# Kernel optimization log

Hardware: AMD Instinct MI355X
Metric: run time of the kernel (lower is better)

Reference implementation:

```python
import jax, jax.numpy as jnp
import numpy as np

B, T, C = 4, 2048, 1024
H = 16
HD = C // H

def setup_inputs() -> dict:
    key = jax.random.key(0)
    k1, k2, k3 = jax.random.split(key, 3)
    x = jax.random.normal(k1, (B, T, C), dtype=jnp.float32)
    w_attn = jax.random.normal(k2, (C, 3 * C), dtype=jnp.float32) * 0.02
    b_attn = jnp.zeros((3 * C,), dtype=jnp.float32)
    w_proj = jax.random.normal(k3, (C, C), dtype=jnp.float32) * 0.02
    b_proj = jnp.zeros((C,), dtype=jnp.float32)
    return {"x": x, "w_attn": w_attn, "b_attn": b_attn, "w_proj": w_proj, "b_proj": b_proj}

def reference(x, w_attn, b_attn, w_proj, b_proj):
    Bx, Tx, Cx = x.shape
    qkv = x @ w_attn + b_attn                      # [B,T,3C]
    q, k, v = jnp.split(qkv, 3, axis=-1)
    # [B,T,C] -> [B,H,T,HD]
    q = q.reshape(Bx, Tx, H, HD).transpose(0, 2, 1, 3)
    k = k.reshape(Bx, Tx, H, HD).transpose(0, 2, 1, 3)
    v = v.reshape(Bx, Tx, H, HD).transpose(0, 2, 1, 3)
    scale = 1.0 / jnp.sqrt(jnp.asarray(HD, dtype=x.dtype))
    att = jnp.einsum('bhqd,bhkd->bhqk', q, k) * scale
    causal = jnp.tril(jnp.ones((Tx, Tx), dtype=bool))
    att = jnp.where(causal[None, None], att, jnp.finfo(att.dtype).min)
    att = jax.nn.softmax(att, axis=-1)
    y = jnp.einsum('bhqk,bhkd->bhqd', att, v)       # [B,H,T,HD]
    y = y.transpose(0, 2, 1, 3).reshape(Bx, Tx, Cx)
    return y @ w_proj + b_proj
```

## Files before the change

kernel.cpp:

```cpp
#include <hip/hip_runtime.h>
#include <hip/hip_bf16.h>

#define B_ 4
#define T_ 2048
#define C_ 1024
#define H_ 16
#define HD_ 64
#define BT_ (B_*T_)
#define C3_ (3*C_)
#define BHTD_ ((size_t)B_*H_*T_*HD_)

#define QSCALE 0.18033688011112042f

using u16 = unsigned short;
using u32 = unsigned int;
using bf16x8 = __attribute__((ext_vector_type(8))) short;
using f32x4  = __attribute__((ext_vector_type(4))) float;
using f32x16 = __attribute__((ext_vector_type(16))) float;
using u16x4  = __attribute__((ext_vector_type(4))) u16;
typedef int i32x2 __attribute__((ext_vector_type(2)));

#if __has_builtin(__builtin_amdgcn_exp2f)
#define EXP2(x) __builtin_amdgcn_exp2f(x)
#else
#define EXP2(x) exp2f(x)
#endif

__device__ __forceinline__ u16 f2bf(float f) {
  u32 u = __float_as_uint(f);
  u += 0x7fffu + ((u >> 16) & 1u);
  return (u16)(u >> 16);
}

__device__ __forceinline__ u32 cvtpk(float lo, float hi) {
  u32 r;
  asm("v_cvt_pk_bf16_f32 %0, %1, %2" : "=v"(r) : "v"(lo), "v"(hi));
  return r;
}

__device__ __forceinline__ void plswap(u32 &a, u32 &b) {
#if __has_builtin(__builtin_amdgcn_permlane32_swap)
  i32x2 r = __builtin_amdgcn_permlane32_swap((int)a, (int)b, false, false);
  a = (u32)r[0]; b = (u32)r[1];
#else
  asm volatile("v_permlane32_swap_b32 %0, %1" : "+v"(a), "+v"(b));
#endif
}

__device__ __forceinline__ float xmaxf(float x) {
  u32 a = __float_as_uint(x), b = a;
  plswap(a, b);
  return fmaxf(__uint_as_float(a), __uint_as_float(b));
}
__device__ __forceinline__ float xaddf(float x) {
  u32 a = __float_as_uint(x), b = a;
  plswap(a, b);
  return __uint_as_float(a) + __uint_as_float(b);
}

__device__ __forceinline__ void gload16(const void* g,
                                        __attribute__((address_space(3))) void* l) {
  __builtin_amdgcn_global_load_lds((const __attribute__((address_space(1))) void*)g,
                                   l, 16, 0, 0);
}

__global__ __launch_bounds__(256) void k_cvt_bf16(const float* __restrict__ in,
                                                  u16* __restrict__ out) {
  size_t i = (size_t)(blockIdx.x * blockDim.x + threadIdx.x) * 4;
  f32x4 f = *(const f32x4*)(in + i);
  u16x4 o;
  o[0] = f2bf(f[0]); o[1] = f2bf(f[1]); o[2] = f2bf(f[2]); o[3] = f2bf(f[3]);
  *(u16x4*)(out + i) = o;
}

__global__ __launch_bounds__(256) void k_transpose_bf16(const float* __restrict__ w,
                                                        u16* __restrict__ wt,
                                                        int K, int N) {
  __shared__ float t[32][33];
  int n0 = blockIdx.x * 32, k0 = blockIdx.y * 32;
  int tx = threadIdx.x & 31;
  int ty = threadIdx.x >> 5;
  #pragma unroll
  for (int r = 0; r < 4; ++r)
    t[ty + r*8][tx] = w[(size_t)(k0 + ty + r*8) * N + n0 + tx];
  __syncthreads();
  #pragma unroll
  for (int r = 0; r < 4; ++r)
    wt[(size_t)(n0 + ty + r*8) * K + k0 + tx] = f2bf(t[tx][ty + r*8]);
}

__global__ __launch_bounds__(256) void k_transpose_v(const u16* __restrict__ src,
                                                     u16* __restrict__ dst) {
  __shared__ u16 t[64][72];
  int bh = blockIdx.y;
  int t0 = blockIdx.x * 64;
  const u16* s = src + (size_t)bh * T_ * HD_;
  u16* d = dst + (size_t)bh * HD_ * T_;
  int r = threadIdx.x >> 2, c0 = (threadIdx.x & 3) * 16;
  bf16x8 a0 = *(const bf16x8*)(s + (size_t)(t0 + r)*HD_ + c0);
  bf16x8 a1 = *(const bf16x8*)(s + (size_t)(t0 + r)*HD_ + c0 + 8);
  #pragma unroll
  for (int j = 0; j < 8; ++j) t[r][c0 + j] = (u16)a0[j];
  #pragma unroll
  for (int j = 0; j < 8; ++j) t[r][c0 + 8 + j] = (u16)a1[j];
  __syncthreads();
  bf16x8 b0, b1;
  #pragma unroll
  for (int j = 0; j < 8; ++j) b0[j] = (short)t[c0 + j][r];
  #pragma unroll
  for (int j = 0; j < 8; ++j) b1[j] = (short)t[c0 + 8 + j][r];
  *(bf16x8*)(d + (size_t)r*T_ + t0 + c0) = b0;
  *(bf16x8*)(d + (size_t)r*T_ + t0 + c0 + 8) = b1;
}

template<int EPI>
__global__ __launch_bounds__(256) void k_gemm(const u16* __restrict__ A,
                                              const u16* __restrict__ Bt,
                                              const float* __restrict__ bias,
                                              void* __restrict__ outp,
                                              void* __restrict__ outp2,
                                              int K) {
  __shared__ __align__(16) u16 lA[128*32];
  __shared__ __align__(16) u16 lB[128*32];
  int tid = threadIdx.x;
  int wave = tid >> 6, lane = tid & 63;
  int wr = wave >> 1, wc = wave & 1;
  int lrow = lane & 15, lgrp = lane >> 4;
  int nwg = gridDim.x * gridDim.y;
  int bidf = blockIdx.y * gridDim.x + blockIdx.x;
  int swzb = (bidf & 7) * (nwg >> 3) + (bidf >> 3);
  int bx = swzb % gridDim.x, by = swzb / gridDim.x;
  int row0 = by * 128, col0 = bx * 128;

  f32x4 zero = {0.f, 0.f, 0.f, 0.f};
  f32x4 acc[4][4];
  #pragma unroll
  for (int m = 0; m < 4; ++m)
    #pragma unroll
    for (int n = 0; n < 4; ++n) acc[m][n] = zero;

  for (int kt = 0; kt < K; kt += 32) {
    #pragma unroll
    for (int p = 0; p < 2; ++p) {
      int c = (wave*2 + p)*64 + lane;
      int r = c >> 2, kc = c & 3;
      int sk = kc ^ ((r >> 1) & 3);
      gload16(A  + (size_t)(row0 + r)*K + kt + sk*8,
              (__attribute__((address_space(3))) char*)lA + (wave*2 + p)*1024);
      gload16(Bt + (size_t)(col0 + r)*K + kt + sk*8,
              (__attribute__((address_space(3))) char*)lB + (wave*2 + p)*1024);
    }
    __syncthreads();
    bf16x8 af[4], bfr[4];
    #pragma unroll
    for (int m = 0; m < 4; ++m) {
      int row = wr*64 + m*16 + lrow;
      af[m] = *(const bf16x8*)(lA + row*32 + (lgrp ^ ((row >> 1) & 3))*8);
    }
    #pragma unroll
    for (int n = 0; n < 4; ++n) {
      int row = wc*64 + n*16 + lrow;
      bfr[n] = *(const bf16x8*)(lB + row*32 + (lgrp ^ ((row >> 1) & 3))*8);
    }
    #pragma unroll
    for (int m = 0; m < 4; ++m)
      #pragma unroll
      for (int n = 0; n < 4; ++n)
        acc[m][n] = __builtin_amdgcn_mfma_f32_16x16x32_bf16(af[m], bfr[n], acc[m][n], 0, 0, 0);
    __syncthreads();
  }

  #pragma unroll
  for (int m = 0; m < 4; ++m) {
    #pragma unroll
    for (int n = 0; n < 4; ++n) {
      int gcol = col0 + wc*64 + n*16 + lrow;
      float bv = bias[gcol];
      #pragma unroll
      for (int r = 0; r < 4; ++r) {
        int grow = row0 + wr*64 + m*16 + lgrp*4 + r;
        float val = acc[m][n][r] + bv;
        if (EPI == 0) {
          int which = gcol >> 10, c = gcol & 1023;
          int hh = c >> 6, d = c & 63;
          int bb = grow >> 11, tt = grow & 2047;
          if (which == 0) val *= QSCALE;
          size_t idx = ((size_t)(bb*H_ + hh)*T_ + tt)*HD_ + d;
          if (which == 2)
            ((u16*)outp2)[idx] = f2bf(val);
          else
            ((u16*)outp)[(size_t)which*BHTD_ + idx] = f2bf(val);
        } else {
          ((float*)outp)[(size_t)grow*C_ + gcol] = val;
        }
      }
    }
  }
}

__global__ __launch_bounds__(256, 2) void k_attn(const u16* __restrict__ q,
                                                 const u16* __restrict__ k,
                                                 const u16* __restrict__ vt,
                                                 u16* __restrict__ y) {
  int tid = threadIdx.x;
  int wave = tid >> 6, lane = tid & 63;
  int l31 = lane & 31, hi = lane >> 5;
  int bid = blockIdx.x;
  int head = bid & 63;
  int g = bid >> 6;
  int s = (g < 4) ? (g*4 + wave) : (31 - (g - 4)*4 - wave);
  int bidx = head >> 4, hh = head & 15;
  const u16* qb = q  + (size_t)head * T_ * HD_;
  const u16* kb = k  + (size_t)head * T_ * HD_;
  const u16* vb = vt + (size_t)head * HD_ * T_;

  f32x16 zero16 = {0.f,0.f,0.f,0.f,0.f,0.f,0.f,0.f,0.f,0.f,0.f,0.f,0.f,0.f,0.f,0.f};

  int qr0 = s * 64;
  bf16x8 qfA[4], qfB[4];
  {
    const u16* qrowA = qb + (size_t)(qr0 + l31)*HD_ + hi*8;
    const u16* qrowB = qrowA + 32*HD_;
    #pragma unroll
    for (int i = 0; i < 4; ++i) { qfA[i] = *(const bf16x8*)(qrowA + 16*i);
                                  qfB[i] = *(const bf16x8*)(qrowB + 16*i); }
  }

  f32x16 oA0 = zero16, oA1 = zero16, oB0 = zero16, oB1 = zero16;
  float mrunA = -1e30f, lrunA = 0.f, mrunB = -1e30f, lrunB = 0.f;
  int qgA = qr0 + l31, qgB = qr0 + 32 + l31;

  auto halfstep = [&](bf16x8 (&qf)[4], f32x16 &od0, f32x16 &od1,
                      float &mrun, float &lrun, int qg, int kv0, bool domask,
                      bf16x8 (&kf)[8], bf16x8 (&vf)[8]) {
    f32x16 s0 = zero16, s1 = zero16;
    __builtin_amdgcn_s_setprio(1);
    s0 = __builtin_amdgcn_mfma_f32_32x32x16_bf16(kf[0], qf[0], s0, 0, 0, 0);
    s1 = __builtin_amdgcn_mfma_f32_32x32x16_bf16(kf[4], qf[0], s1, 0, 0, 0);
    s0 = __builtin_amdgcn_mfma_f32_32x32x16_bf16(kf[1], qf[1], s0, 0, 0, 0);
    s1 = __builtin_amdgcn_mfma_f32_32x32x16_bf16(kf[5], qf[1], s1, 0, 0, 0);
    s0 = __builtin_amdgcn_mfma_f32_32x32x16_bf16(kf[2], qf[2], s0, 0, 0, 0);
    s1 = __builtin_amdgcn_mfma_f32_32x32x16_bf16(kf[6], qf[2], s1, 0, 0, 0);
    s0 = __builtin_amdgcn_mfma_f32_32x32x16_bf16(kf[3], qf[3], s0, 0, 0, 0);
    s1 = __builtin_amdgcn_mfma_f32_32x32x16_bf16(kf[7], qf[3], s1, 0, 0, 0);
    __builtin_amdgcn_s_setprio(0);

    if (domask) {
      #pragma unroll
      for (int r = 0; r < 16; ++r) {
        int kl = (r & 3) + 8*(r >> 2) + 4*hi;
        if (kv0 + kl      > qg) s0[r] = -1e30f;
        if (kv0 + 32 + kl > qg) s1[r] = -1e30f;
      }
    }

    float t[16];
    #pragma unroll
    for (int i = 0; i < 16; ++i) t[i] = fmaxf(s0[i], s1[i]);
    #pragma unroll
    for (int off = 8; off > 0; off >>= 1)
      #pragma unroll
      for (int i = 0; i < 8; ++i)
        if (i < off) t[i] = fmaxf(t[i], t[i + off]);
    float pmax = xmaxf(t[0]);

    float mnew = fmaxf(mrun, pmax);
    float ex = EXP2(mrun - mnew);
    mrun = mnew;

    #pragma unroll
    for (int i = 0; i < 16; ++i) s0[i] = EXP2(s0[i] - mnew);
    #pragma unroll
    for (int i = 0; i < 16; ++i) s1[i] = EXP2(s1[i] - mnew);
    float u[16];
    #pragma unroll
    for (int i = 0; i < 16; ++i) u[i] = s0[i] + s1[i];
    #pragma unroll
    for (int off = 8; off > 0; off >>= 1)
      #pragma unroll
      for (int i = 0; i < 8; ++i)
        if (i < off) u[i] = u[i] + u[i + off];
    float rsum = xaddf(u[0]);
    lrun = lrun * ex + rsum;

    #pragma unroll
    for (int i = 0; i < 16; ++i) { od0[i] *= ex; od1[i] *= ex; }

    bf16x8 pf0, pf1, pf2, pf3;
    {
      u32 a0 = cvtpk(s0[0], s0[1]),   a1 = cvtpk(s0[2], s0[3]);
      u32 b0 = cvtpk(s0[4], s0[5]),   b1 = cvtpk(s0[6], s0[7]);
      plswap(a0, b0); plswap(a1, b1);
      u32 wa[4] = {a0, a1, b0, b1};
      __builtin_memcpy(&pf0, wa, 16);
    }
    {
      u32 a0 = cvtpk(s0[8], s0[9]),   a1 = cvtpk(s0[10], s0[11]);
      u32 b0 = cvtpk(s0[12], s0[13]), b1 = cvtpk(s0[14], s0[15]);
      plswap(a0, b0); plswap(a1, b1);
      u32 wa[4] = {a0, a1, b0, b1};
      __builtin_memcpy(&pf1, wa, 16);
    }
    {
      u32 a0 = cvtpk(s1[0], s1[1]),   a1 = cvtpk(s1[2], s1[3]);
      u32 b0 = cvtpk(s1[4], s1[5]),   b1 = cvtpk(s1[6], s1[7]);
      plswap(a0, b0); plswap(a1, b1);
      u32 wa[4] = {a0, a1, b0, b1};
      __builtin_memcpy(&pf2, wa, 16);
    }
    {
      u32 a0 = cvtpk(s1[8], s1[9]),   a1 = cvtpk(s1[10], s1[11]);
      u32 b0 = cvtpk(s1[12], s1[13]), b1 = cvtpk(s1[14], s1[15]);
      plswap(a0, b0); plswap(a1, b1);
      u32 wa[4] = {a0, a1, b0, b1};
      __builtin_memcpy(&pf3, wa, 16);
    }

    __builtin_amdgcn_s_setprio(1);
    od0 = __builtin_amdgcn_mfma_f32_32x32x16_bf16(vf[0], pf0, od0, 0, 0, 0);
    od0 = __builtin_amdgcn_mfma_f32_32x32x16_bf16(vf[1], pf1, od0, 0, 0, 0);
    od0 = __builtin_amdgcn_mfma_f32_32x32x16_bf16(vf[2], pf2, od0, 0, 0, 0);
    od0 = __builtin_amdgcn_mfma_f32_32x32x16_bf16(vf[3], pf3, od0, 0, 0, 0);
    od1 = __builtin_amdgcn_mfma_f32_32x32x16_bf16(vf[4], pf0, od1, 0, 0, 0);
    od1 = __builtin_amdgcn_mfma_f32_32x32x16_bf16(vf[5], pf1, od1, 0, 0, 0);
    od1 = __builtin_amdgcn_mfma_f32_32x32x16_bf16(vf[6], pf2, od1, 0, 0, 0);
    od1 = __builtin_amdgcn_mfma_f32_32x32x16_bf16(vf[7], pf3, od1, 0, 0, 0);
    __builtin_amdgcn_s_setprio(0);
  };

  for (int t = 0; t <= s; ++t) {
    int kv0 = t*64;
    bool last = (t == s);

    bf16x8 kf[8], vf[8];
    {
      const u16* krow = kb + (size_t)(kv0 + l31)*HD_ + hi*8;
      const u16* krow1 = krow + 32*HD_;
      #pragma unroll
      for (int i = 0; i < 4; ++i) { kf[i] = *(const bf16x8*)(krow + 16*i);
                                    kf[4+i] = *(const bf16x8*)(krow1 + 16*i); }
      const u16* vrow = vb + (size_t)l31*T_ + kv0 + hi*8;
      const u16* vrow1 = vrow + 32*T_;
      #pragma unroll
      for (int i = 0; i < 4; ++i) { vf[i] = *(const bf16x8*)(vrow + 16*i);
                                    vf[4+i] = *(const bf16x8*)(vrow1 + 16*i); }
    }

    halfstep(qfA, oA0, oA1, mrunA, lrunA, qgA, kv0, last, kf, vf);
    halfstep(qfB, oB0, oB1, mrunB, lrunB, qgB, kv0, last, kf, vf);
  }

  {
    float inv = 1.0f / lrunA;
    u16* yrow = y + ((size_t)(bidx*T_) + qr0 + l31)*C_ + hh*64;
    #pragma unroll
    for (int r = 0; r < 8; ++r) {
      int dp = ((2*r) & 3) + 8*(r >> 1) + 4*hi;
      *(u32*)(yrow + dp)      = cvtpk(oA0[2*r]*inv, oA0[2*r+1]*inv);
      *(u32*)(yrow + 32 + dp) = cvtpk(oA1[2*r]*inv, oA1[2*r+1]*inv);
    }
  }
  {
    float inv = 1.0f / lrunB;
    u16* yrow = y + ((size_t)(bidx*T_) + qr0 + 32 + l31)*C_ + hh*64;
    #pragma unroll
    for (int r = 0; r < 8; ++r) {
      int dp = ((2*r) & 3) + 8*(r >> 1) + 4*hi;
      *(u32*)(yrow + dp)      = cvtpk(oB0[2*r]*inv, oB0[2*r+1]*inv);
      *(u32*)(yrow + 32 + dp) = cvtpk(oB1[2*r]*inv, oB1[2*r+1]*inv);
    }
  }
}

extern "C" void kernel_launch(void* const* d_in, const int* in_sizes, int n_in,
                              void* d_out, int out_size, void* d_ws, size_t ws_size,
                              hipStream_t stream) {
  const float* x      = (const float*)d_in[0];
  const float* w_attn = (const float*)d_in[1];
  const float* b_attn = (const float*)d_in[2];
  const float* w_proj = (const float*)d_in[3];
  const float* b_proj = (const float*)d_in[4];

  char* ws = (char*)d_ws;
  size_t off = 0;
  auto walloc = [&](size_t bytes) -> void* {
    void* p = ws + off;
    off += (bytes + 255) & ~(size_t)255;
    return p;
  };
  u16* xbf  = (u16*)walloc((size_t)BT_ * C_ * 2);
  u16* wat  = (u16*)walloc((size_t)C3_ * C_ * 2);
  u16* wpt  = (u16*)walloc((size_t)C_ * C_ * 2);
  u16* qkv  = (u16*)walloc(3 * BHTD_ * 2);
  u16* vtmp = (u16*)walloc(BHTD_ * 2);
  u16* qp = qkv;
  u16* kp = qkv + BHTD_;
  u16* vp = qkv + 2*BHTD_;
  u16* ybf = xbf;

  k_cvt_bf16<<<(BT_*C_)/1024, 256, 0, stream>>>(x, xbf);
  k_transpose_bf16<<<dim3(C3_/32, C_/32), 256, 0, stream>>>(w_attn, wat, C_, C3_);
  k_transpose_bf16<<<dim3(C_/32, C_/32), 256, 0, stream>>>(w_proj, wpt, C_, C_);
  k_gemm<0><<<dim3(C3_/128, BT_/128), 256, 0, stream>>>(xbf, wat, b_attn, (void*)qkv, (void*)vtmp, C_);
  k_transpose_v<<<dim3(T_/64, B_*H_), 256, 0, stream>>>(vtmp, vp);
  k_attn<<<dim3(512), 256, 0, stream>>>(qp, kp, vp, ybf);
  k_gemm<1><<<dim3(C_/128, BT_/128), 256, 0, stream>>>(ybf, wpt, b_proj, d_out, nullptr, C_);
}
```

Measured before the change: 194.8 us.

## Split attention KV loop across wave pairs with LDS softmax merge

Each attention block now has 8 waves instead of 4. Each query tile is handled by a pair of waves, and each wave processes half of the causal KV range. Per-block query tiles are paired so that total work per block is balanced. The two partial softmax states (running max, running sum, output accumulators) are merged through shared memory before writing. This doubles the wave-level parallelism for the same 512 blocks. The cost is extra synchronisation, LDS traffic and more register pressure from the launch_bounds(512,4) request.

```diff
diff --git a/kernel.cpp b/kernel.cpp
--- a/kernel.cpp
+++ b/kernel.cpp
@@ -198,17 +198,19 @@
   }
 }
 
-__global__ __launch_bounds__(256, 2) void k_attn(const u16* __restrict__ q,
+__global__ __launch_bounds__(512, 4) void k_attn(const u16* __restrict__ q,
                                                  const u16* __restrict__ k,
                                                  const u16* __restrict__ vt,
                                                  u16* __restrict__ y) {
+  __shared__ float mlds[4][64][34];
   int tid = threadIdx.x;
   int wave = tid >> 6, lane = tid & 63;
   int l31 = lane & 31, hi = lane >> 5;
   int bid = blockIdx.x;
   int head = bid & 63;
-  int g = bid >> 6;
-  int s = (g < 4) ? (g*4 + wave) : (31 - (g - 4)*4 - wave);
+  int p = bid >> 6;
+  int pair = wave >> 1, half = wave & 1;
+  int s = (pair == 0) ? p : (pair == 1) ? (15 - p) : (pair == 2) ? (31 - p) : (16 + p);
   int bidx = head >> 4, hh = head & 15;
   const u16* qb = q  + (size_t)head * T_ * HD_;
   const u16* kb = k  + (size_t)head * T_ * HD_;
@@ -328,7 +330,10 @@
     __builtin_amdgcn_s_setprio(0);
   };
 
-  for (int t = 0; t <= s; ++t) {
+  int nt = s + 1;
+  int tbeg = half ? (nt >> 1) : 0;
+  int tend = half ? nt : (nt >> 1);
+  for (int t = tbeg; t < tend; ++t) {
     int kv0 = t*64;
     bool last = (t == s);
 
@@ -350,24 +355,54 @@
     halfstep(qfB, oB0, oB1, mrunB, lrunB, qgB, kv0, last, kf, vf);
   }
 
-  {
-    float inv = 1.0f / lrunA;
+  float* mybuf = &mlds[pair][lane][0];
+
+  if (half) {
+    #pragma unroll
+    for (int i = 0; i < 16; ++i) { mybuf[i] = oA0[i]; mybuf[16 + i] = oA1[i]; }
+    mybuf[32] = mrunA; mybuf[33] = lrunA;
+  }
+  __syncthreads();
+  if (!half) {
+    float mb = mybuf[32], lb = mybuf[33];
+    float m = fmaxf(mrunA, mb);
+    float ea = EXP2(mrunA - m), eb = EXP2(mb - m);
+    float inv = 1.0f / (lrunA*ea + lb*eb);
     u16* yrow = y + ((size_t)(bidx*T_) + qr0 + l31)*C_ + hh*64;
     #pragma unroll
     for (int r = 0; r < 8; ++r) {
       int dp = ((2*r) & 3) + 8*(r >> 1) + 4*hi;
-      *(u32*)(yrow + dp)      = cvtpk(oA0[2*r]*inv, oA0[2*r+1]*inv);
-      *(u32*)(yrow + 32 + dp) = cvtpk(oA1[2*r]*inv, oA1[2*r+1]*inv);
-    }
-  }
-  {
-    float inv = 1.0f / lrunB;
+      float a0 = (oA0[2*r]*ea   + mybuf[2*r]*eb)      * inv;
+      float a1 = (oA0[2*r+1]*ea + mybuf[2*r+1]*eb)    * inv;
+      float b0 = (oA1[2*r]*ea   + mybuf[16+2*r]*eb)   * inv;
+      float b1 = (oA1[2*r+1]*ea + mybuf[16+2*r+1]*eb) * inv;
+      *(u32*)(yrow + dp)      = cvtpk(a0, a1);
+      *(u32*)(yrow + 32 + dp) = cvtpk(b0, b1);
+    }
+  }
+  __syncthreads();
+
+  if (half) {
+    #pragma unroll
+    for (int i = 0; i < 16; ++i) { mybuf[i] = oB0[i]; mybuf[16 + i] = oB1[i]; }
+    mybuf[32] = mrunB; mybuf[33] = lrunB;
+  }
+  __syncthreads();
+  if (!half) {
+    float mb = mybuf[32], lb = mybuf[33];
+    float m = fmaxf(mrunB, mb);
+    float ea = EXP2(mrunB - m), eb = EXP2(mb - m);
+    float inv = 1.0f / (lrunB*ea + lb*eb);
     u16* yrow = y + ((size_t)(bidx*T_) + qr0 + 32 + l31)*C_ + hh*64;
     #pragma unroll
     for (int r = 0; r < 8; ++r) {
       int dp = ((2*r) & 3) + 8*(r >> 1) + 4*hi;
-      *(u32*)(yrow + dp)      = cvtpk(oB0[2*r]*inv, oB0[2*r+1]*inv);
-      *(u32*)(yrow + 32 + dp) = cvtpk(oB1[2*r]*inv, oB1[2*r+1]*inv);
+      float a0 = (oB0[2*r]*ea   + mybuf[2*r]*eb)      * inv;
+      float a1 = (oB0[2*r+1]*ea + mybuf[2*r+1]*eb)    * inv;
+      float b0 = (oB1[2*r]*ea   + mybuf[16+2*r]*eb)   * inv;
+      float b1 = (oB1[2*r+1]*ea + mybuf[16+2*r+1]*eb) * inv;
+      *(u32*)(yrow + dp)      = cvtpk(a0, a1);
+      *(u32*)(yrow + 32 + dp) = cvtpk(b0, b1);
     }
   }
 }
@@ -403,6 +438,6 @@
   k_transpose_bf16<<<dim3(C_/32, C_/32), 256, 0, stream>>>(w_proj, wpt, C_, C_);
   k_gemm<0><<<dim3(C3_/128, BT_/128), 256, 0, stream>>>(xbf, wat, b_attn, (void*)qkv, (void*)vtmp, C_);
   k_transpose_v<<<dim3(T_/64, B_*H_), 256, 0, stream>>>(vtmp, vp);
-  k_attn<<<dim3(512), 256, 0, stream>>>(qp, kp, vp, ybf);
+  k_attn<<<dim3(512), 512, 0, stream>>>(qp, kp, vp, ybf);
   k_gemm<1><<<dim3(C_/128, BT_/128), 256, 0, stream>>>(ybf, wpt, b_proj, d_out, nullptr, C_);
 }
```

Measured after the change: 503.0 us. +158.3%, slower.
